# Optimization experiments

Hardware: AMD Instinct MI355X
Metric: run time of the kernel (lower is better)

Reference implementation:

```python
import jax, jax.numpy as jnp
import numpy as np

KERNEL_SIZE = 4
SCALE_FACTOR = 0.5


def setup_inputs() -> dict:
    key = jax.random.key(0)
    k1, k2, k3 = jax.random.split(key, 3)
    batch, in_f, out_f = 4096, 2048, 4096
    x = jax.random.normal(k1, (batch, in_f), dtype=jnp.float32)
    # kaiming-uniform-like scale for weights
    W = jax.random.normal(k2, (out_f, in_f), dtype=jnp.float32) * (1.0 / np.sqrt(in_f))
    b = jax.random.normal(k3, (out_f,), dtype=jnp.float32) * (1.0 / np.sqrt(in_f))
    return {"x": x, "W": W, "b": b}


def reference(x, W, b):
    # Linear: (B, out_f)
    y = jnp.einsum("bi,oi->bo", x, W) + b
    B, out_f = y.shape
    groups = out_f // KERNEL_SIZE
    # MaxPool1d(kernel_size, stride=kernel_size) over feature dim
    pooled = jnp.max(y.reshape(B, groups, KERNEL_SIZE), axis=-1)  # (B, groups)
    # sum over pooled features, then scale -> (B,)
    return jnp.sum(pooled, axis=-1) * SCALE_FACTOR
```

## Files before the change

### kernel.cpp

```cpp
#include <hip/hip_runtime.h>


typedef float  f32x4   __attribute__((ext_vector_type(4)));
typedef short  bf16x8  __attribute__((ext_vector_type(8)));
typedef short  short4v __attribute__((ext_vector_type(4)));

__device__ __forceinline__ short f2bf(float f) {
    union { float f; unsigned u; } v; v.f = f;
    unsigned r = v.u + 0x7FFFu + ((v.u >> 16) & 1u);
    return (short)(r >> 16);
}

__global__ void cvt_kernel(const float* __restrict__ x, const float* __restrict__ w,
                           short* __restrict__ out, long nx, long nw) {
    long total4 = (nx + nw) >> 2;
    long stride = (long)gridDim.x * blockDim.x;
    for (long i = (long)blockIdx.x * blockDim.x + threadIdx.x; i < total4; i += stride) {
        long e = i << 2;
        const float* src = (e < nx) ? (x + e) : (w + (e - nx));
        float4 v = *(const float4*)src;
        short4v s = { f2bf(v.x), f2bf(v.y), f2bf(v.z), f2bf(v.w) };
        *(short4v*)(out + e) = s;
    }
}

#define LDSOFF(rc, q) ((((rc) >> 3) << 9) + (((rc) & 7) << 6) + ((((q) ^ ((rc) & 7))) << 3))

__device__ __forceinline__ void stage_A(const short* __restrict__ G, short* lds,
                                        int blockRow, int K, int kt, int half,
                                        int wid, int lane) {
#pragma unroll
    for (int i = 0; i < 2; ++i) {
        int idx = wid * 2 + i;
        int c   = (idx & 7) + ((idx >> 3) << 4) + (half << 3);
        int row = (c << 3) + (lane >> 3);
        int q   = (lane & 7) ^ (lane >> 3);
        const short* src = G + (size_t)(blockRow + row) * K + kt * 64 + q * 8;
        __builtin_amdgcn_global_load_lds(
            (const __attribute__((address_space(1))) unsigned int*)src,
            (__attribute__((address_space(3))) unsigned int*)(lds + c * 512),
            16, 0, 0);
    }
}

__device__ __forceinline__ void stage_B(const short* __restrict__ G, short* lds,
                                        int blockCol, int K, int kt, int half,
                                        int wid, int lane) {
#pragma unroll
    for (int i = 0; i < 2; ++i) {
        int idx = wid * 2 + i;
        int c   = ((idx >> 2) << 3) + (idx & 3) + (half << 2);
        int row = (c << 3) + (lane >> 3);
        int q   = (lane & 7) ^ (lane >> 3);
        const short* src = G + (size_t)(blockCol + row) * K + kt * 64 + q * 8;
        __builtin_amdgcn_global_load_lds(
            (const __attribute__((address_space(1))) unsigned int*)src,
            (__attribute__((address_space(3))) unsigned int*)(lds + c * 512),
            16, 0, 0);
    }
}

__global__ __launch_bounds__(512, 2) void gemm_pool_kernel(
    const short* __restrict__ X, const short* __restrict__ W,
    const float* __restrict__ bias, float* __restrict__ out, int K)
{
    __shared__ short As[32768];
    __shared__ short Bs[32768];

    const int tid  = threadIdx.x;
    const int lane = tid & 63;
    const int wid  = tid >> 6;
    const int wr   = wid >> 2;
    const int wc   = wid & 3;
    const int hi   = lane >> 4;
    const int lo   = lane & 15;

    const int nwg  = gridDim.x * gridDim.y;
    const int bid  = blockIdx.y * gridDim.x + blockIdx.x;
    const int wgid = (bid & 7) * (nwg >> 3) + (bid >> 3);
    const int brow = (wgid / gridDim.x) * 256;
    const int bcol = (wgid % gridDim.x) * 256;
    const int nk   = K >> 6;

    f32x4 acc[8][4] = {};
    bf16x8 a0[4][2], a1[4][2], b0[2][2], b1[2][2];

    stage_A(X, As,         brow, K, 0, 0, wid, lane);
    stage_B(W, Bs,         bcol, K, 0, 0, wid, lane);
    stage_B(W, Bs,         bcol, K, 0, 1, wid, lane);
    stage_A(X, As,         brow, K, 0, 1, wid, lane);
    stage_A(X, As + 16384, brow, K, 1, 0, wid, lane);
    stage_B(W, Bs + 16384, bcol, K, 1, 1, wid, lane);
    stage_A(X, As + 16384, brow, K, 1, 1, wid, lane);
    asm volatile("s_waitcnt vmcnt(6)" ::: "memory");
    __builtin_amdgcn_s_barrier();

    for (int t = 0; t < nk; ++t) {
        short* Ab = As + ((t & 1) << 14);
        short* Bb = Bs + ((t & 1) << 14);
        short* Bn = Bs + (((t & 1) ^ 1) << 14);

#pragma unroll
        for (int mm = 0; mm < 4; ++mm)
#pragma unroll
            for (int kk = 0; kk < 2; ++kk) {
                int rc = wr * 128 + mm * 16 + lo;
                a0[mm][kk] = *(const bf16x8*)(Ab + LDSOFF(rc, kk * 4 + hi));
            }
#pragma unroll
        for (int nn = 0; nn < 2; ++nn)
#pragma unroll
            for (int kk = 0; kk < 2; ++kk) {
                int rc = wc * 64 + nn * 16 + lo;
                b0[nn][kk] = *(const bf16x8*)(Bb + LDSOFF(rc, kk * 4 + hi));
            }
        if (t + 1 < nk) stage_B(W, Bn, bcol, K, t + 1, 0, wid, lane);
        __builtin_amdgcn_s_barrier();
#pragma unroll
        for (int nn = 0; nn < 2; ++nn)
#pragma unroll
            for (int kk = 0; kk < 2; ++kk) {
                int rc = wc * 64 + 32 + nn * 16 + lo;
                b1[nn][kk] = *(const bf16x8*)(Bb + LDSOFF(rc, kk * 4 + hi));
            }
        __builtin_amdgcn_s_setprio(1);
#pragma unroll
        for (int mm = 0; mm < 4; ++mm)
#pragma unroll
            for (int nn = 0; nn < 2; ++nn)
#pragma unroll
                for (int kk = 0; kk < 2; ++kk)
                    acc[mm][nn] = __builtin_amdgcn_mfma_f32_16x16x32_bf16(
                        a0[mm][kk], b0[nn][kk], acc[mm][nn], 0, 0, 0);
        __builtin_amdgcn_s_setprio(0);

        __builtin_amdgcn_s_barrier();
#pragma unroll
        for (int mm = 0; mm < 4; ++mm)
#pragma unroll
            for (int kk = 0; kk < 2; ++kk) {
                int rc = wr * 128 + 64 + mm * 16 + lo;
                a1[mm][kk] = *(const bf16x8*)(Ab + LDSOFF(rc, kk * 4 + hi));
            }
        if (t + 2 < nk) stage_A(X, Ab, brow, K, t + 2, 0, wid, lane);
        __builtin_amdgcn_s_setprio(1);
#pragma unroll
        for (int mm = 0; mm < 4; ++mm)
#pragma unroll
            for (int nn = 0; nn < 2; ++nn)
#pragma unroll
                for (int kk = 0; kk < 2; ++kk)
                    acc[mm][2 + nn] = __builtin_amdgcn_mfma_f32_16x16x32_bf16(
                        a0[mm][kk], b1[nn][kk], acc[mm][2 + nn], 0, 0, 0);
        __builtin_amdgcn_s_setprio(0);

        __builtin_amdgcn_s_barrier();
        if (t + 2 < nk) stage_B(W, Bb, bcol, K, t + 2, 1, wid, lane);
        __builtin_amdgcn_s_setprio(1);
#pragma unroll
        for (int mm = 0; mm < 4; ++mm)
#pragma unroll
            for (int nn = 0; nn < 2; ++nn)
#pragma unroll
                for (int kk = 0; kk < 2; ++kk)
                    acc[4 + mm][2 + nn] = __builtin_amdgcn_mfma_f32_16x16x32_bf16(
                        a1[mm][kk], b1[nn][kk], acc[4 + mm][2 + nn], 0, 0, 0);
        __builtin_amdgcn_s_setprio(0);

        __builtin_amdgcn_s_barrier();
        if (t + 2 < nk) stage_A(X, Ab, brow, K, t + 2, 1, wid, lane);
        __builtin_amdgcn_s_setprio(1);
#pragma unroll
        for (int mm = 0; mm < 4; ++mm)
#pragma unroll
            for (int nn = 0; nn < 2; ++nn)
#pragma unroll
                for (int kk = 0; kk < 2; ++kk)
                    acc[4 + mm][nn] = __builtin_amdgcn_mfma_f32_16x16x32_bf16(
                        a1[mm][kk], b0[nn][kk], acc[4 + mm][nn], 0, 0, 0);
        __builtin_amdgcn_s_setprio(0);
        if (t == nk - 2)      asm volatile("s_waitcnt vmcnt(0)" ::: "memory");
        else if (t < nk - 2)  asm volatile("s_waitcnt vmcnt(6)" ::: "memory");
        __builtin_amdgcn_s_barrier();
    }

    float bias_n[4];
#pragma unroll
    for (int nn = 0; nn < 4; ++nn)
        bias_n[nn] = bias[bcol + wc * 64 + nn * 16 + lo];

#pragma unroll
    for (int mm = 0; mm < 8; ++mm) {
#pragma unroll
        for (int j = 0; j < 4; ++j) {
            float part = 0.f;
#pragma unroll
            for (int nn = 0; nn < 4; ++nn) {
                float v = acc[mm][nn][j] + bias_n[nn];
                v = fmaxf(v, __shfl_xor(v, 1));
                v = fmaxf(v, __shfl_xor(v, 2));
                part += v;
            }
            part += __shfl_xor(part, 4);
            part += __shfl_xor(part, 8);
            if (lo == 0)
                atomicAdd(&out[brow + wr * 128 + mm * 16 + hi * 4 + j], part * 0.5f);
        }
    }
}

extern "C" void kernel_launch(void* const* d_in, const int* in_sizes, int n_in,
                              void* d_out, int out_size, void* d_ws, size_t ws_size,
                              hipStream_t stream) {
    const float* x = (const float*)d_in[0];
    const float* W = (const float*)d_in[1];
    const float* b = (const float*)d_in[2];
    float* out = (float*)d_out;

    const int N = in_sizes[2];
    const int K = in_sizes[1] / N;
    const int M = in_sizes[0] / K;

    hipMemsetAsync(out, 0, (size_t)out_size * sizeof(float), stream);

    short* xb = (short*)d_ws;
    short* wb = xb + in_sizes[0];
    cvt_kernel<<<2048, 256, 0, stream>>>(x, W, (short*)d_ws,
                                         (long)in_sizes[0], (long)in_sizes[1]);

    dim3 grid(N / 256, M / 256);
    gemm_pool_kernel<<<grid, 512, 0, stream>>>(xb, wb, b, out, K);
}
```

Baseline: 97.29 us.

## Switch GEMM inner loop to 32x32x16 bf16 MFMA tiles

Replaces the 16x16x32 MFMA tiling with 32x32x16 MFMA instructions, so each wave now holds a 4x2 grid of 16-wide f32 accumulators. The LDS fragment loads, the phase schedule with extra barriers, and the pooled epilogue are rebuilt to match the 32x32 output layout, with an extra shuffle level and new row indexing. The aim is fewer MFMA issues and fewer LDS reads per FLOP, since larger MFMAs give more reuse per operand. In exchange there are extra barriers per iteration and register pressure may change.

Result: slower. 121.5 us (+24.9%).

```diff
diff --git a/kernel.cpp b/kernel.cpp
--- a/kernel.cpp
+++ b/kernel.cpp
@@ -1,7 +1,7 @@
 #include <hip/hip_runtime.h>
 
 
-typedef float  f32x4   __attribute__((ext_vector_type(4)));
+typedef float  f32x16  __attribute__((ext_vector_type(16)));
 typedef short  bf16x8  __attribute__((ext_vector_type(8)));
 typedef short  short4v __attribute__((ext_vector_type(4)));
 
@@ -72,8 +72,8 @@
     const int wid  = tid >> 6;
     const int wr   = wid >> 2;
     const int wc   = wid & 3;
-    const int hi   = lane >> 4;
-    const int lo   = lane & 15;
+    const int lo32 = lane & 31;
+    const int hi32 = lane >> 5;
 
     const int nwg  = gridDim.x * gridDim.y;
     const int bid  = blockIdx.y * gridDim.x + blockIdx.x;
@@ -82,8 +82,8 @@
     const int bcol = (wgid % gridDim.x) * 256;
     const int nk   = K >> 6;
 
-    f32x4 acc[8][4] = {};
-    bf16x8 a0[4][2], a1[4][2], b0[2][2], b1[2][2];
+    f32x16 acc[4][2] = {};
+    bf16x8 a[2][4], b[4];
 
     stage_A(X, As,         brow, K, 0, 0, wid, lane);
     stage_B(W, Bs,         bcol, K, 0, 0, wid, lane);
@@ -101,110 +101,104 @@
         short* Bn = Bs + (((t & 1) ^ 1) << 14);
 
 #pragma unroll
-        for (int mm = 0; mm < 4; ++mm)
-#pragma unroll
-            for (int kk = 0; kk < 2; ++kk) {
-                int rc = wr * 128 + mm * 16 + lo;
-                a0[mm][kk] = *(const bf16x8*)(Ab + LDSOFF(rc, kk * 4 + hi));
+        for (int mi = 0; mi < 2; ++mi)
+#pragma unroll
+            for (int ks = 0; ks < 4; ++ks) {
+                int rc = wr * 128 + mi * 32 + lo32;
+                a[mi][ks] = *(const bf16x8*)(Ab + LDSOFF(rc, ks * 2 + hi32));
             }
 #pragma unroll
-        for (int nn = 0; nn < 2; ++nn)
-#pragma unroll
-            for (int kk = 0; kk < 2; ++kk) {
-                int rc = wc * 64 + nn * 16 + lo;
-                b0[nn][kk] = *(const bf16x8*)(Bb + LDSOFF(rc, kk * 4 + hi));
+        for (int ks = 0; ks < 4; ++ks) {
+            int rc = wc * 64 + lo32;
+            b[ks] = *(const bf16x8*)(Bb + LDSOFF(rc, ks * 2 + hi32));
+        }
+        if (t + 1 < nk) stage_B(W, Bn, bcol, K, t + 1, 0, wid, lane);
+        __builtin_amdgcn_s_barrier();
+        __builtin_amdgcn_s_setprio(1);
+#pragma unroll
+        for (int ks = 0; ks < 4; ++ks) {
+            acc[0][0] = __builtin_amdgcn_mfma_f32_32x32x16_bf16(a[0][ks], b[ks], acc[0][0], 0, 0, 0);
+            acc[1][0] = __builtin_amdgcn_mfma_f32_32x32x16_bf16(a[1][ks], b[ks], acc[1][0], 0, 0, 0);
+        }
+        __builtin_amdgcn_s_setprio(0);
+        __builtin_amdgcn_s_barrier();
+
+#pragma unroll
+        for (int ks = 0; ks < 4; ++ks) {
+            int rc = wc * 64 + 32 + lo32;
+            b[ks] = *(const bf16x8*)(Bb + LDSOFF(rc, ks * 2 + hi32));
+        }
+        if (t + 2 < nk) stage_A(X, Ab, brow, K, t + 2, 0, wid, lane);
+        __builtin_amdgcn_s_barrier();
+        __builtin_amdgcn_s_setprio(1);
+#pragma unroll
+        for (int ks = 0; ks < 4; ++ks) {
+            acc[0][1] = __builtin_amdgcn_mfma_f32_32x32x16_bf16(a[0][ks], b[ks], acc[0][1], 0, 0, 0);
+            acc[1][1] = __builtin_amdgcn_mfma_f32_32x32x16_bf16(a[1][ks], b[ks], acc[1][1], 0, 0, 0);
+        }
+        __builtin_amdgcn_s_setprio(0);
+        __builtin_amdgcn_s_barrier();
+
+#pragma unroll
+        for (int mi = 0; mi < 2; ++mi)
+#pragma unroll
+            for (int ks = 0; ks < 4; ++ks) {
+                int rc = wr * 128 + 64 + mi * 32 + lo32;
+                a[mi][ks] = *(const bf16x8*)(Ab + LDSOFF(rc, ks * 2 + hi32));
             }
-        if (t + 1 < nk) stage_B(W, Bn, bcol, K, t + 1, 0, wid, lane);
-        __builtin_amdgcn_s_barrier();
-#pragma unroll
-        for (int nn = 0; nn < 2; ++nn)
-#pragma unroll
-            for (int kk = 0; kk < 2; ++kk) {
-                int rc = wc * 64 + 32 + nn * 16 + lo;
-                b1[nn][kk] = *(const bf16x8*)(Bb + LDSOFF(rc, kk * 4 + hi));
-            }
-        __builtin_amdgcn_s_setprio(1);
-#pragma unroll
-        for (int mm = 0; mm < 4; ++mm)
-#pragma unroll
-            for (int nn = 0; nn < 2; ++nn)
-#pragma unroll
-                for (int kk = 0; kk < 2; ++kk)
-                    acc[mm][nn] = __builtin_amdgcn_mfma_f32_16x16x32_bf16(
-                        a0[mm][kk], b0[nn][kk], acc[mm][nn], 0, 0, 0);
-        __builtin_amdgcn_s_setprio(0);
-
-        __builtin_amdgcn_s_barrier();
-#pragma unroll
-        for (int mm = 0; mm < 4; ++mm)
-#pragma unroll
-            for (int kk = 0; kk < 2; ++kk) {
-                int rc = wr * 128 + 64 + mm * 16 + lo;
-                a1[mm][kk] = *(const bf16x8*)(Ab + LDSOFF(rc, kk * 4 + hi));
-            }
-        if (t + 2 < nk) stage_A(X, Ab, brow, K, t + 2, 0, wid, lane);
-        __builtin_amdgcn_s_setprio(1);
-#pragma unroll
-        for (int mm = 0; mm < 4; ++mm)
-#pragma unroll
-            for (int nn = 0; nn < 2; ++nn)
-#pragma unroll
-                for (int kk = 0; kk < 2; ++kk)
-                    acc[mm][2 + nn] = __builtin_amdgcn_mfma_f32_16x16x32_bf16(
-                        a0[mm][kk], b1[nn][kk], acc[mm][2 + nn], 0, 0, 0);
-        __builtin_amdgcn_s_setprio(0);
-
-        __builtin_amdgcn_s_barrier();
         if (t + 2 < nk) stage_B(W, Bb, bcol, K, t + 2, 1, wid, lane);
-        __builtin_amdgcn_s_setprio(1);
-#pragma unroll
-        for (int mm = 0; mm < 4; ++mm)
-#pragma unroll
-            for (int nn = 0; nn < 2; ++nn)
-#pragma unroll
-                for (int kk = 0; kk < 2; ++kk)
-                    acc[4 + mm][2 + nn] = __builtin_amdgcn_mfma_f32_16x16x32_bf16(
-                        a1[mm][kk], b1[nn][kk], acc[4 + mm][2 + nn], 0, 0, 0);
-        __builtin_amdgcn_s_setprio(0);
-
-        __builtin_amdgcn_s_barrier();
+        __builtin_amdgcn_s_barrier();
+        __builtin_amdgcn_s_setprio(1);
+#pragma unroll
+        for (int ks = 0; ks < 4; ++ks) {
+            acc[2][1] = __builtin_amdgcn_mfma_f32_32x32x16_bf16(a[0][ks], b[ks], acc[2][1], 0, 0, 0);
+            acc[3][1] = __builtin_amdgcn_mfma_f32_32x32x16_bf16(a[1][ks], b[ks], acc[3][1], 0, 0, 0);
+        }
+        __builtin_amdgcn_s_setprio(0);
+        __builtin_amdgcn_s_barrier();
+
+#pragma unroll
+        for (int ks = 0; ks < 4; ++ks) {
+            int rc = wc * 64 + lo32;
+            b[ks] = *(const bf16x8*)(Bb + LDSOFF(rc, ks * 2 + hi32));
+        }
         if (t + 2 < nk) stage_A(X, Ab, brow, K, t + 2, 1, wid, lane);
-        __builtin_amdgcn_s_setprio(1);
-#pragma unroll
-        for (int mm = 0; mm < 4; ++mm)
-#pragma unroll
-            for (int nn = 0; nn < 2; ++nn)
-#pragma unroll
-                for (int kk = 0; kk < 2; ++kk)
-                    acc[4 + mm][nn] = __builtin_amdgcn_mfma_f32_16x16x32_bf16(
-                        a1[mm][kk], b0[nn][kk], acc[4 + mm][nn], 0, 0, 0);
+        __builtin_amdgcn_s_barrier();
+        __builtin_amdgcn_s_setprio(1);
+#pragma unroll
+        for (int ks = 0; ks < 4; ++ks) {
+            acc[2][0] = __builtin_amdgcn_mfma_f32_32x32x16_bf16(a[0][ks], b[ks], acc[2][0], 0, 0, 0);
+            acc[3][0] = __builtin_amdgcn_mfma_f32_32x32x16_bf16(a[1][ks], b[ks], acc[3][0], 0, 0, 0);
+        }
         __builtin_amdgcn_s_setprio(0);
         if (t == nk - 2)      asm volatile("s_waitcnt vmcnt(0)" ::: "memory");
         else if (t < nk - 2)  asm volatile("s_waitcnt vmcnt(6)" ::: "memory");
         __builtin_amdgcn_s_barrier();
     }
 
-    float bias_n[4];
-#pragma unroll
-    for (int nn = 0; nn < 4; ++nn)
-        bias_n[nn] = bias[bcol + wc * 64 + nn * 16 + lo];
-
-#pragma unroll
-    for (int mm = 0; mm < 8; ++mm) {
-#pragma unroll
-        for (int j = 0; j < 4; ++j) {
+    float bias_n[2];
+#pragma unroll
+    for (int nn = 0; nn < 2; ++nn)
+        bias_n[nn] = bias[bcol + wc * 64 + nn * 32 + lo32];
+
+#pragma unroll
+    for (int mm = 0; mm < 4; ++mm) {
+#pragma unroll
+        for (int r = 0; r < 16; ++r) {
             float part = 0.f;
 #pragma unroll
-            for (int nn = 0; nn < 4; ++nn) {
-                float v = acc[mm][nn][j] + bias_n[nn];
+            for (int nn = 0; nn < 2; ++nn) {
+                float v = acc[mm][nn][r] + bias_n[nn];
                 v = fmaxf(v, __shfl_xor(v, 1));
                 v = fmaxf(v, __shfl_xor(v, 2));
                 part += v;
             }
             part += __shfl_xor(part, 4);
             part += __shfl_xor(part, 8);
-            if (lo == 0)
-                atomicAdd(&out[brow + wr * 128 + mm * 16 + hi * 4 + j], part * 0.5f);
+            part += __shfl_xor(part, 16);
+            if (lo32 == 0)
+                atomicAdd(&out[brow + wr * 128 + mm * 32 +
+                               (r & 3) + 8 * (r >> 2) + 4 * hi32], part * 0.5f);
         }
     }
 }
```
